# Kernel tuning notes

Hardware: AMD Instinct MI355X
Metric: run time of the kernel (lower is better)

Reference implementation:

```python
import jax, jax.numpy as jnp
import numpy as np

CATS = [1000, 1000, 2000]
NDS = len(CATS)
TOT = sum(CATS)          # total_cats = 4000
N = TOT + NDS            # 4003 source (label) nodes
U = 2048                 # num_unify_class
NFEAT = 256
F = 256                  # nfeat_out
OUT_FEAT = 512           # output_feat_dim
ADJ_FEAT = 256           # adj_feat_dim
SINKHORN_ITERS = 20


def setup_inputs() -> dict:
    key = jax.random.key(0)
    ks = jax.random.split(key, 16)

    def rn(k, shape, s):
        return jax.random.normal(k, shape, dtype=jnp.float32) * s

    return {
        "datasets_node_features": jax.random.normal(ks[0], (TOT, NFEAT), dtype=jnp.float32),
        "unlable_node_features": rn(ks[1], (NDS, NFEAT), 0.02),  # trunc_normal_(std=0.02)
        "adj_matrix": jax.random.uniform(ks[2], (N, U), dtype=jnp.float32),  # torch.rand init
        "W_before": rn(ks[3], (NFEAT, F), 0.05), "b_before": jnp.zeros((F,), jnp.float32),
        "gc1_W": rn(ks[4], (F, F), 0.05), "gc1_b": jnp.zeros((F,), jnp.float32),
        "gc2_W": rn(ks[5], (F, F), 0.05), "gc2_b": jnp.zeros((F,), jnp.float32),
        "gc3_W": rn(ks[6], (F, F), 0.05), "gc3_b": jnp.zeros((F,), jnp.float32),
        "W1": rn(ks[7], (F, OUT_FEAT), 0.05), "b1": jnp.zeros((OUT_FEAT,), jnp.float32),
        "W2": rn(ks[8], (OUT_FEAT, ADJ_FEAT), 0.05), "b2": jnp.zeros((ADJ_FEAT,), jnp.float32),
    }


def _log_optimal_transport(scores, iters):
    # log-space Sinkhorn with uniform marginals 1/(m+n), then rescale by (m+n)
    m, n = scores.shape
    norm = -jnp.log(jnp.asarray(m + n, scores.dtype))
    log_mu = jnp.full((m,), norm, scores.dtype)
    log_nu = jnp.full((n,), norm, scores.dtype)

    def body(carry, _):
        u, v = carry
        u = log_mu - jax.nn.logsumexp(scores + v[None, :], axis=1)
        v = log_nu - jax.nn.logsumexp(scores + u[:, None], axis=0)
        return (u, v), None

    (u, v), _ = jax.lax.scan(body, (jnp.zeros_like(log_mu), jnp.zeros_like(log_nu)),
                             None, length=iters)
    return scores + u[:, None] + v[None, :] - norm


def reference(datasets_node_features, unlable_node_features, adj_matrix,
              W_before, b_before, gc1_W, gc1_b, gc2_W, gc2_b, gc3_W, gc3_b,
              W1, b1, W2, b2):
    # node features: dataset class nodes + per-dataset 'unlabeled' nodes -> [N, NFEAT]
    feats = jnp.concatenate([datasets_node_features, unlable_node_features], axis=0)
    x = jax.nn.relu(feats @ W_before + b_before)  # [N, F]

    # learnable adjacency normalized via differentiable Sinkhorn OT  [N, U]
    A = jnp.exp(_log_optimal_transport(adj_matrix, SINKHORN_ITERS))

    # bipartite message passing: full graph adj has zero diagonal blocks,
    # so spmm(adj, h) splits into A @ h_u (into label nodes) and A.T @ h_n (into unify nodes).
    hn = x                 # [N, F] label-node features
    hu = A.T @ x           # [U, F] initial unify-node features via aggregation

    def gcn(hn, hu, W, b):
        # GraphConvolution: spmm(adj, h @ W) + b ; GCN wrapper: tanh(out + h)
        new_n = jnp.tanh(A @ (hu @ W) + b + hn)
        new_u = jnp.tanh(A.T @ (hn @ W) + b + hu)
        return new_n, new_u

    hn, hu = gcn(hn, hu, gc1_W, gc1_b)
    hn, hu = gcn(hn, hu, gc2_W, gc2_b)
    hn, hu = gcn(hn, hu, gc3_W, gc3_b)

    # output head on unify nodes: linear1 -> relu -> linear2  [U, ADJ_FEAT]
    out = jax.nn.relu(hu @ W1 + b1) @ W2 + b2
    return out
```

## Files before the change

kernel.cpp:

```cpp
#include <hip/hip_runtime.h>
#include <hip/hip_fp16.h>
#include <math.h>

#define NN 4003
#define UU 2048
#define KP 4032
#define N4P 4004
#define NORMC (-8.7079796f)

using bf16x8 = __attribute__((ext_vector_type(8))) short;
using f32x4  = __attribute__((ext_vector_type(4))) float;

#define GLL16(g, l) __builtin_amdgcn_global_load_lds( \
    (const __attribute__((address_space(1))) unsigned*)(g), \
    (__attribute__((address_space(3))) unsigned*)(l), 16, 0, 0)

__device__ __forceinline__ ushort f2bf(float x) {
    unsigned u = __builtin_bit_cast(unsigned, x);
    u += 0x7fff + ((u >> 16) & 1);
    return (ushort)(u >> 16);
}
__device__ __forceinline__ float bf2f(ushort h) {
    unsigned u = ((unsigned)h) << 16;
    return __builtin_bit_cast(float, u);
}
__device__ __forceinline__ void bfsplit(float x, ushort& hi, ushort& lo) {
    hi = f2bf(x);
    lo = f2bf(x - bf2f(hi));
}
__device__ __forceinline__ float h2f(ushort h) {
    return __half2float(__ushort_as_half(h));
}

__global__ void concat_bf(const float* __restrict__ a, const float* __restrict__ b,
                          ushort* __restrict__ fh, ushort* __restrict__ fl) {
    int i = blockIdx.x * 256 + threadIdx.x;
    const int tot4 = NN * 256 / 4;
    if (i >= tot4) return;
    float4 v = (i < 256000) ? ((const float4*)a)[i] : ((const float4*)b)[i - 256000];
    ushort4 hv, lv;
    bfsplit(v.x, hv.x, lv.x); bfsplit(v.y, hv.y, lv.y);
    bfsplit(v.z, hv.z, lv.z); bfsplit(v.w, hv.w, lv.w);
    *(ushort4*)(fh + ((size_t)i << 2)) = hv;
    *(ushort4*)(fl + ((size_t)i << 2)) = lv;
}

__global__ void convW(const float* __restrict__ W, ushort* __restrict__ Th,
                      ushort* __restrict__ Tl, int K, int Nw) {
    __shared__ float tile[32][33];
    int bx = blockIdx.x, by = blockIdx.y;
    int tx = threadIdx.x;
    for (int r = threadIdx.y; r < 32; r += 8)
        tile[r][tx] = W[(size_t)(by * 32 + r) * Nw + bx * 32 + tx];
    __syncthreads();
    for (int r = threadIdx.y; r < 32; r += 8) {
        int n = bx * 32 + r, k = by * 32 + tx;
        ushort hi, lo; bfsplit(tile[tx][r], hi, lo);
        Th[(size_t)n * K + k] = hi;
        Tl[(size_t)n * K + k] = lo;
    }
}

__global__ void conv_sh(const float* __restrict__ S, ushort* __restrict__ Sh) {
    int i = blockIdx.x * 256 + threadIdx.x;
    const int tot4 = NN * UU / 4;
    if (i >= tot4) return;
    float4 s = ((const float4*)S)[i];
    ushort4 h;
    h.x = __half_as_ushort(__float2half(s.x));
    h.y = __half_as_ushort(__float2half(s.y));
    h.z = __half_as_ushort(__float2half(s.z));
    h.w = __half_as_ushort(__float2half(s.w));
    *(ushort4*)(Sh + ((size_t)i << 2)) = h;
}

__global__ void transpose_h(const float* __restrict__ in, ushort* __restrict__ out) {
    __shared__ float tile[32][33];
    int x = blockIdx.x * 32 + threadIdx.x;
    int y0 = blockIdx.y * 32;
    for (int r = threadIdx.y; r < 32; r += 8) {
        int y = y0 + r;
        tile[r][threadIdx.x] = (y < NN) ? in[(size_t)y * UU + x] : 0.0f;
    }
    __syncthreads();
    int oc = y0 + threadIdx.x;
    for (int r = threadIdx.y; r < 32; r += 8) {
        int orow = blockIdx.x * 32 + r;
        out[(size_t)orow * KP + oc] = __half_as_ushort(__float2half(tile[threadIdx.x][r]));
    }
}

__global__ void init_uext(float* __restrict__ u_ext) {
    int i = threadIdx.x;
    if (i < KP - NN) u_ext[NN + i] = -1e30f;
}

__global__ __launch_bounds__(256) void lse2h(const ushort* __restrict__ Sh, int lda,
                                             const float* __restrict__ addv,
                                             float* __restrict__ outv, int C, int R) {
    int r0 = blockIdx.x * 2, r1 = r0 + 1;
    bool has1 = (r1 < R);
    const ushort* rowa = Sh + (size_t)r0 * lda;
    const ushort* rowb = Sh + (size_t)(has1 ? r1 : r0) * lda;
    const float4* a4 = (const float4*)addv;
    float m0 = -INFINITY, s0 = 0.0f, m1 = -INFINITY, s1 = 0.0f;
    int C4 = C >> 2;
    for (int j = threadIdx.x; j < C4; j += 256) {
        float4 av = a4[j];
        ushort4 pa = *(const ushort4*)(rowa + (j << 2));
        ushort4 pb = *(const ushort4*)(rowb + (j << 2));
        float a0 = h2f(pa.x) + av.x, a1 = h2f(pa.y) + av.y;
        float a2 = h2f(pa.z) + av.z, a3 = h2f(pa.w) + av.w;
        float b0 = h2f(pb.x) + av.x, b1 = h2f(pb.y) + av.y;
        float b2 = h2f(pb.z) + av.z, b3 = h2f(pb.w) + av.w;
        float mxa = fmaxf(fmaxf(a0, a1), fmaxf(a2, a3));
        float nm0 = fmaxf(m0, mxa);
        s0 = s0 * __expf(m0 - nm0) + __expf(a0 - nm0) + __expf(a1 - nm0)
                                   + __expf(a2 - nm0) + __expf(a3 - nm0);
        m0 = nm0;
        float mxb = fmaxf(fmaxf(b0, b1), fmaxf(b2, b3));
        float nm1 = fmaxf(m1, mxb);
        s1 = s1 * __expf(m1 - nm1) + __expf(b0 - nm1) + __expf(b1 - nm1)
                                   + __expf(b2 - nm1) + __expf(b3 - nm1);
        m1 = nm1;
    }
    int rem = C & 3;
    if ((int)threadIdx.x < rem) {
        int j = (C4 << 2) + threadIdx.x;
        float av = addv[j];
        float xa = h2f(rowa[j]) + av;
        float nm0 = fmaxf(m0, xa);
        s0 = s0 * __expf(m0 - nm0) + __expf(xa - nm0);
        m0 = nm0;
        float xb = h2f(rowb[j]) + av;
        float nm1 = fmaxf(m1, xb);
        s1 = s1 * __expf(m1 - nm1) + __expf(xb - nm1);
        m1 = nm1;
    }
    #pragma unroll
    for (int off = 1; off < 64; off <<= 1) {
        float om = __shfl_xor(m0, off, 64), os = __shfl_xor(s0, off, 64);
        float nm = fmaxf(m0, om);
        s0 = s0 * __expf(m0 - nm) + os * __expf(om - nm);
        m0 = nm;
        om = __shfl_xor(m1, off, 64); os = __shfl_xor(s1, off, 64);
        nm = fmaxf(m1, om);
        s1 = s1 * __expf(m1 - nm) + os * __expf(om - nm);
        m1 = nm;
    }
    __shared__ float sm[8], ss[8];
    int w = threadIdx.x >> 6;
    if ((threadIdx.x & 63) == 0) { sm[w] = m0; ss[w] = s0; sm[4 + w] = m1; ss[4 + w] = s1; }
    __syncthreads();
    if (threadIdx.x < 2) {
        int b = threadIdx.x * 4;
        float m = sm[b], s = ss[b];
        #pragma unroll
        for (int i = 1; i < 4; ++i) {
            float om = sm[b + i], os = ss[b + i];
            float nm = fmaxf(m, om);
            s = s * __expf(m - nm) + os * __expf(om - nm);
            m = nm;
        }
        int r = r0 + threadIdx.x;
        if (threadIdx.x == 0 || has1) outv[r] = NORMC - (m + __logf(s));
    }
}

__device__ __forceinline__ void exp_row8h(const ushort* __restrict__ Sh,
        const float* __restrict__ rowadd, const float* __restrict__ coladd,
        int lda, int M, int gm, int kbase, uint4& hiv, uint4& lov) {
    ushort h[8], l[8];
    if (gm < M) {
        float ra = rowadd[gm] - NORMC;
        const ushort* rp = Sh + (size_t)gm * lda + kbase;
        ushort4 q0 = *(const ushort4*)rp;
        ushort4 q1 = *(const ushort4*)(rp + 4);
        float4 ca = *(const float4*)(coladd + kbase);
        float4 cb = *(const float4*)(coladd + kbase + 4);
        float vv[8] = {h2f(q0.x) + ca.x, h2f(q0.y) + ca.y, h2f(q0.z) + ca.z, h2f(q0.w) + ca.w,
                       h2f(q1.x) + cb.x, h2f(q1.y) + cb.y, h2f(q1.z) + cb.z, h2f(q1.w) + cb.w};
        #pragma unroll
        for (int e = 0; e < 8; ++e) {
            float av = __expf(vv[e] + ra);
            bfsplit(av, h[e], l[e]);
        }
    } else {
        #pragma unroll
        for (int e = 0; e < 8; ++e) { h[e] = 0; l[e] = 0; }
    }
    hiv.x = (unsigned)h[0] | ((unsigned)h[1] << 16);
    hiv.y = (unsigned)h[2] | ((unsigned)h[3] << 16);
    hiv.z = (unsigned)h[4] | ((unsigned)h[5] << 16);
    hiv.w = (unsigned)h[6] | ((unsigned)h[7] << 16);
    lov.x = (unsigned)l[0] | ((unsigned)l[1] << 16);
    lov.y = (unsigned)l[2] | ((unsigned)l[3] << 16);
    lov.z = (unsigned)l[4] | ((unsigned)l[5] << 16);
    lov.w = (unsigned)l[6] | ((unsigned)l[7] << 16);
}

__global__ __launch_bounds__(512) __attribute__((amdgpu_waves_per_eu(2, 4)))
void gemm_bigN(
        const ushort* __restrict__ Sh, const float* __restrict__ rowadd,
        const float* __restrict__ coladd, int lda,
        const ushort* __restrict__ Bh, const ushort* __restrict__ Bl, int ldb,
        float* __restrict__ P, int M, int K, int Kc) {
    __shared__ __align__(16) ushort SM[2 * 64 * 64 + 2 * 256 * 64];
    ushort* As0 = SM;
    ushort* As1 = SM + 4096;
    ushort* Bs0 = SM + 8192;
    ushort* Bs1 = SM + 8192 + 16384;
    const int tid = threadIdx.x;
    const int bm = blockIdx.x << 6;
    const int lane = tid & 63;
    const int wv = tid >> 6;
    const int wr = (wv >> 2) << 5;
    const int wc = (wv & 3) << 6;
    const int kb = blockIdx.y * Kc;
    int ke = kb + Kc; if (ke > K) ke = K;
    const int arow = tid >> 3, ak8 = (tid & 7) << 3;
    const int as = ((arow << 6) + ak8) ^ ((arow & 7) << 3);
    const int brow_base = wv << 5;
    f32x4 acc[2][4] = {};
    for (int k0 = kb; k0 < ke; k0 += 64) {
        uint4 ah, al;
        exp_row8h(Sh, rowadd, coladd, lda, M, bm + arow, k0 + ak8, ah, al);
        __syncthreads();
        #pragma unroll
        for (int t = 0; t < 4; ++t) {
            int rb2 = brow_base + (t << 3);
            int row = rb2 + (lane >> 3);
            int kksrc = (((lane & 7) ^ (row & 7)) << 3);
            size_t go = (size_t)row * ldb + k0 + kksrc;
            GLL16(Bh + go, &Bs0[rb2 << 6]);
            GLL16(Bl + go, &Bs1[rb2 << 6]);
        }
        *(uint4*)&As0[as] = ah;
        *(uint4*)&As1[as] = al;
        __syncthreads();
        #pragma unroll
        for (int ks = 0; ks < 2; ++ks) {
            int kq = (ks << 5) + ((lane >> 4) << 3);
            bf16x8 fah[2], fal[2], fbh[4], fbl[4];
            #pragma unroll
            for (int f = 0; f < 2; ++f) {
                int rr = wr + (f << 4) + (lane & 15);
                int ia = ((rr << 6) + kq) ^ ((rr & 7) << 3);
                fah[f] = *(const bf16x8*)&As0[ia];
                fal[f] = *(const bf16x8*)&As1[ia];
            }
            #pragma unroll
            for (int g = 0; g < 4; ++g) {
                int cc = wc + (g << 4) + (lane & 15);
                int ib = ((cc << 6) + kq) ^ ((cc & 7) << 3);
                fbh[g] = *(const bf16x8*)&Bs0[ib];
                fbl[g] = *(const bf16x8*)&Bs1[ib];
            }
            #pragma unroll
            for (int i = 0; i < 2; ++i)
                #pragma unroll
                for (int j = 0; j < 4; ++j) {
                    acc[i][j] = __builtin_amdgcn_mfma_f32_16x16x32_bf16(fah[i], fbh[j], acc[i][j], 0, 0, 0);
                    acc[i][j] = __builtin_amdgcn_mfma_f32_16x16x32_bf16(fah[i], fbl[j], acc[i][j], 0, 0, 0);
                    acc[i][j] = __builtin_amdgcn_mfma_f32_16x16x32_bf16(fal[i], fbh[j], acc[i][j], 0, 0, 0);
                }
        }
    }
    __syncthreads();
    float* LF = (float*)SM;
    #pragma unroll
    for (int i = 0; i < 2; ++i) {
        int row0 = wr + (i << 4) + ((lane >> 4) << 2);
        #pragma unroll
        for (int j = 0; j < 4; ++j) {
            int col = wc + (j << 4) + (lane & 15);
            #pragma unroll
            for (int r = 0; r < 4; ++r)
                LF[(row0 + r) * 256 + col] = acc[i][j][r];
        }
    }
    __syncthreads();
    float* Pp = P + (size_t)blockIdx.y * ((size_t)M * 256);
    #pragma unroll
    for (int it = 0; it < 8; ++it) {
        int idx = tid + (it << 9);
        int row = idx >> 6, c4 = (idx & 63) << 2;
        if (bm + row < M)
            *(float4*)(Pp + (size_t)(bm + row) * 256 + c4) = *(const float4*)&LF[row * 256 + c4];
    }
}

__global__ __launch_bounds__(256) __attribute__((amdgpu_waves_per_eu(4, 8)))
void gemm_ks(
        const ushort* __restrict__ Ah, const ushort* __restrict__ Al, int lda,
        const ushort* __restrict__ Bh, const ushort* __restrict__ Bl, int ldb, int Nb,
        float* __restrict__ P, int M, int Nplane, int K, int Kc) {
    __shared__ __align__(16) ushort SM[4 * 64 * 64];
    ushort* As0 = SM;
    ushort* As1 = SM + 4096;
    ushort* Bs0 = SM + 8192;
    ushort* Bs1 = SM + 12288;
    const int tid = threadIdx.x;
    const int bm = blockIdx.y << 6, bn = blockIdx.x << 6;
    const int lane = tid & 63;
    const int wv = tid >> 6;
    const int wm = (wv >> 1) << 5, wn = (wv & 1) << 5;
    const int kb = blockIdx.z * Kc;
    int ke = kb + Kc; if (ke > K) ke = K;
    const int rb = wv << 4;
    f32x4 acc[2][2] = {};
    for (int k0 = kb; k0 < ke; k0 += 64) {
        __syncthreads();
        #pragma unroll
        for (int t = 0; t < 2; ++t) {
            int rb2 = rb + (t << 3);
            int row = rb2 + (lane >> 3);
            int kksrc = (((lane & 7) ^ (row & 7)) << 3);
            int ga = bm + row; ga = (ga < M) ? ga : (M - 1);
            int gb = bn + row; gb = (gb < Nb) ? gb : (Nb - 1);
            size_t goa = (size_t)ga * lda + k0 + kksrc;
            size_t gob = (size_t)gb * ldb + k0 + kksrc;
            GLL16(Ah + goa, &As0[rb2 << 6]);
            GLL16(Al + goa, &As1[rb2 << 6]);
            GLL16(Bh + gob, &Bs0[rb2 << 6]);
            GLL16(Bl + gob, &Bs1[rb2 << 6]);
        }
        __syncthreads();
        #pragma unroll
        for (int ks = 0; ks < 2; ++ks) {
            int kbq = (ks << 5) + ((lane >> 4) << 3);
            bf16x8 fah[2], fal[2], fbh[2], fbl[2];
            #pragma unroll
            for (int f = 0; f < 2; ++f) {
                int rr = wm + (f << 4) + (lane & 15);
                int ia = ((rr << 6) + kbq) ^ ((rr & 7) << 3);
                fah[f] = *(const bf16x8*)&As0[ia];
                fal[f] = *(const bf16x8*)&As1[ia];
                int cc = wn + (f << 4) + (lane & 15);
                int ib = ((cc << 6) + kbq) ^ ((cc & 7) << 3);
                fbh[f] = *(const bf16x8*)&Bs0[ib];
                fbl[f] = *(const bf16x8*)&Bs1[ib];
            }
            #pragma unroll
            for (int i = 0; i < 2; ++i)
                #pragma unroll
                for (int j = 0; j < 2; ++j) {
                    acc[i][j] = __builtin_amdgcn_mfma_f32_16x16x32_bf16(fah[i], fbh[j], acc[i][j], 0, 0, 0);
                    acc[i][j] = __builtin_amdgcn_mfma_f32_16x16x32_bf16(fah[i], fbl[j], acc[i][j], 0, 0, 0);
                    acc[i][j] = __builtin_amdgcn_mfma_f32_16x16x32_bf16(fal[i], fbh[j], acc[i][j], 0, 0, 0);
                }
        }
    }
    __syncthreads();
    float* LF = (float*)SM;
    #pragma unroll
    for (int i = 0; i < 2; ++i) {
        int row0 = wm + (i << 4) + ((lane >> 4) << 2);
        #pragma unroll
        for (int j = 0; j < 2; ++j) {
            int col = wn + (j << 4) + (lane & 15);
            #pragma unroll
            for (int r = 0; r < 4; ++r)
                LF[(row0 + r) * 64 + col] = acc[i][j][r];
        }
    }
    __syncthreads();
    float* Pp = P + (size_t)blockIdx.z * ((size_t)M * Nplane);
    #pragma unroll
    for (int it = 0; it < 4; ++it) {
        int idx = tid + (it << 8);
        int row = idx >> 4, c4 = (idx & 15) << 2;
        if (bm + row < M && bn + c4 < Nplane)
            *(float4*)(Pp + (size_t)(bm + row) * Nplane + bn + c4) = *(const float4*)&LF[row * 64 + c4];
    }
}

template<int ACT, int BIAS, int RES, int OUTK>
__global__ __launch_bounds__(256) void reduce_ks(
        const float* __restrict__ P, int zg,
        const float* __restrict__ bias,
        const ushort* __restrict__ Rh, const ushort* __restrict__ Rl,
        float* __restrict__ Cf, ushort* __restrict__ Ch, ushort* __restrict__ Cl,
        int M, int N4, int ldo) {
    int t = blockIdx.x * 256 + threadIdx.x;
    int n4w = N4 >> 2;
    int tot = M * n4w;
    if (t >= tot) return;
    int m = t / n4w;
    int n = (t - m * n4w) << 2;
    size_t pstr = (size_t)M * N4;
    const float* base = P + (size_t)m * N4 + n;
    float4 a = *(const float4*)base;
    for (int z = 1; z < zg; ++z) {
        float4 b = *(const float4*)(base + (size_t)z * pstr);
        a.x += b.x; a.y += b.y; a.z += b.z; a.w += b.w;
    }
    if (BIAS == 1) {
        float4 bv = *(const float4*)(bias + n);
        a.x += bv.x; a.y += bv.y; a.z += bv.z; a.w += bv.w;
    }
    if (BIAS == 2) {
        float s = bias[m];
        a.x += s; a.y += s; a.z += s; a.w += s;
    }
    if (RES) {
        size_t ro = (size_t)m * ldo + n;
        ushort4 rh = *(const ushort4*)(Rh + ro);
        ushort4 rl = *(const ushort4*)(Rl + ro);
        a.x += bf2f(rh.x) + bf2f(rl.x); a.y += bf2f(rh.y) + bf2f(rl.y);
        a.z += bf2f(rh.z) + bf2f(rl.z); a.w += bf2f(rh.w) + bf2f(rl.w);
    }
    if (ACT == 1) {
        a.x = fmaxf(a.x, 0.f); a.y = fmaxf(a.y, 0.f);
        a.z = fmaxf(a.z, 0.f); a.w = fmaxf(a.w, 0.f);
    }
    if (ACT == 2) {
        a.x = tanhf(a.x); a.y = tanhf(a.y); a.z = tanhf(a.z); a.w = tanhf(a.w);
    }
    size_t co = (size_t)m * ldo + n;
    if (OUTK == 0) {
        *(float4*)(Cf + co) = a;
    } else {
        ushort4 hv, lv;
        bfsplit(a.x, hv.x, lv.x); bfsplit(a.y, hv.y, lv.y);
        bfsplit(a.z, hv.z, lv.z); bfsplit(a.w, hv.w, lv.w);
        *(ushort4*)(Ch + co) = hv;
        *(ushort4*)(Cl + co) = lv;
    }
}

static inline int rgrid(int M, int N4) { return (M * (N4 >> 2) + 255) / 256; }

extern "C" void kernel_launch(void* const* d_in, const int* in_sizes, int n_in,
                              void* d_out, int out_size, void* d_ws, size_t ws_size,
                              hipStream_t stream) {
    const float* dsf = (const float*)d_in[0];
    const float* unl = (const float*)d_in[1];
    const float* S   = (const float*)d_in[2];
    const float* Wb  = (const float*)d_in[3];
    const float* bb  = (const float*)d_in[4];
    const float* gcW[3] = {(const float*)d_in[5], (const float*)d_in[7], (const float*)d_in[9]};
    const float* gcb[3] = {(const float*)d_in[6], (const float*)d_in[8], (const float*)d_in[10]};
    const float* W1 = (const float*)d_in[11];
    const float* b1 = (const float*)d_in[12];
    const float* W2 = (const float*)d_in[13];
    const float* b2 = (const float*)d_in[14];
    float* out = (float*)d_out;

    char* p = (char*)d_ws;
    ushort* Shm = (ushort*)p; p += (size_t)NN * UU * 2;
    ushort* STh = (ushort*)p; p += (size_t)UU * KP * 2;
    float* P    = (float*)p;  p += (size_t)8 * NN * 256 * 4;
    ushort* fh = (ushort*)p; ushort* fl = fh + (size_t)NN * 256; p += (size_t)NN * 256 * 4;
    ushort* xh = (ushort*)p; ushort* xl = xh + (size_t)NN * 256; p += (size_t)NN * 256 * 4;
    ushort* xTh = (ushort*)p; ushort* xTl = xTh + (size_t)256 * KP; p += (size_t)256 * KP * 4;
    ushort* huh = (ushort*)p; ushort* hul = huh + (size_t)UU * 256; p += (size_t)UU * 256 * 4;
    ushort* tuTh = (ushort*)p; ushort* tuTl = tuTh + (size_t)256 * UU; p += (size_t)256 * UU * 4;
    ushort* tnTh = (ushort*)p; ushort* tnTl = tnTh + (size_t)256 * KP; p += (size_t)256 * KP * 4;
    float* u_ext = (float*)p; p += KP * 4;
    float* v     = (float*)p; p += UU * 4;
    ushort* WbTh = (ushort*)p; ushort* WbTl = WbTh + 256 * 256; p += 256 * 256 * 4;
    ushort* gWh[3]; ushort* gWl[3];
    for (int l = 0; l < 3; ++l) { gWh[l] = (ushort*)p; gWl[l] = gWh[l] + 256 * 256; p += 256 * 256 * 4; }
    ushort* W1Th = (ushort*)p; ushort* W1Tl = W1Th + 512 * 256; p += 512 * 256 * 4;
    ushort* W2Th = (ushort*)p; ushort* W2Tl = W2Th + 256 * 512; p += 256 * 512 * 4;
    ushort* h1h = xh; ushort* h1l = h1h + (size_t)UU * 512;
    (void)ws_size;

    concat_bf<<<dim3(1001), dim3(256), 0, stream>>>(dsf, unl, fh, fl);
    convW<<<dim3(8, 8),  dim3(32, 8), 0, stream>>>(Wb, WbTh, WbTl, 256, 256);
    for (int l = 0; l < 3; ++l)
        convW<<<dim3(8, 8), dim3(32, 8), 0, stream>>>(gcW[l], gWh[l], gWl[l], 256, 256);
    convW<<<dim3(16, 8), dim3(32, 8), 0, stream>>>(W1, W1Th, W1Tl, 256, 512);
    convW<<<dim3(8, 16), dim3(32, 8), 0, stream>>>(W2, W2Th, W2Tl, 512, 256);
    init_uext<<<dim3(1), dim3(64), 0, stream>>>(u_ext);
    conv_sh<<<dim3((NN * UU / 4 + 255) / 256), dim3(256), 0, stream>>>(S, Shm);
    transpose_h<<<dim3(64, 126), dim3(32, 8), 0, stream>>>(S, STh);
    hipMemsetAsync(v, 0, UU * sizeof(float), stream);

    gemm_ks<<<dim3(4, 63, 4), 256, 0, stream>>>(
        fh, fl, 256, WbTh, WbTl, 256, 256, P, NN, 256, 256, 64);
    reduce_ks<1,1,0,1><<<rgrid(NN,256), 256, 0, stream>>>(
        P, 4, bb, nullptr, nullptr, nullptr, xh, xl, NN, 256, 256);
    gemm_ks<<<dim3(63, 4, 4), 256, 0, stream>>>(
        WbTh, WbTl, 256, fh, fl, 256, NN, P, 256, N4P, 256, 64);
    reduce_ks<1,2,0,1><<<rgrid(256,N4P), 256, 0, stream>>>(
        P, 4, bb, nullptr, nullptr, nullptr, xTh, xTl, 256, N4P, KP);

    for (int it = 0; it < 20; ++it) {
        lse2h<<<dim3((NN + 1) / 2), dim3(256), 0, stream>>>(Shm, UU, v, u_ext, UU, NN);
        lse2h<<<dim3(UU / 2),       dim3(256), 0, stream>>>(STh, KP, u_ext, v, NN, UU);
    }

    gemm_bigN<<<dim3(32, 8), 512, 0, stream>>>(
        STh, v, u_ext, KP, xTh, xTl, KP, P, UU, KP, 512);
    reduce_ks<0,0,0,1><<<rgrid(UU,256), 256, 0, stream>>>(
        P, 8, nullptr, nullptr, nullptr, nullptr, huh, hul, UU, 256, 256);

    for (int l = 0; l < 3; ++l) {
        const ushort* hnh = (l == 0) ? xh : fh;
        const ushort* hnl = (l == 0) ? xl : fl;
        if (l < 2) {
            gemm_ks<<<dim3(32, 4, 4), 256, 0, stream>>>(
                gWh[l], gWl[l], 256, huh, hul, 256, UU, P, 256, UU, 256, 64);
            reduce_ks<0,0,0,1><<<rgrid(256,UU), 256, 0, stream>>>(
                P, 4, nullptr, nullptr, nullptr, nullptr, tuTh, tuTl, 256, UU, UU);
        }
        gemm_ks<<<dim3(63, 4, 4), 256, 0, stream>>>(
            gWh[l], gWl[l], 256, hnh, hnl, 256, NN, P, 256, N4P, 256, 64);
        reduce_ks<0,0,0,1><<<rgrid(256,N4P), 256, 0, stream>>>(
            P, 4, nullptr, nullptr, nullptr, nullptr, tnTh, tnTl, 256, N4P, KP);
        if (l < 2) {
            gemm_bigN<<<dim3(63, 8), 512, 0, stream>>>(
                Shm, u_ext, v, UU, tuTh, tuTl, UU, P, NN, UU, 256);
            reduce_ks<2,1,1,1><<<rgrid(NN,256), 256, 0, stream>>>(
                P, 8, gcb[l], hnh, hnl, nullptr, fh, fl, NN, 256, 256);
        }
        gemm_bigN<<<dim3(32, 8), 512, 0, stream>>>(
            STh, v, u_ext, KP, tnTh, tnTl, KP, P, UU, KP, 512);
        reduce_ks<2,1,1,1><<<rgrid(UU,256), 256, 0, stream>>>(
            P, 8, gcb[l], huh, hul, nullptr, huh, hul, UU, 256, 256);
    }

    gemm_ks<<<dim3(8, 32, 4), 256, 0, stream>>>(
        huh, hul, 256, W1Th, W1Tl, 256, 512, P, UU, 512, 256, 64);
    reduce_ks<1,1,0,1><<<rgrid(UU,512), 256, 0, stream>>>(
        P, 4, b1, nullptr, nullptr, nullptr, h1h, h1l, UU, 512, 512);
    gemm_ks<<<dim3(4, 32, 8), 256, 0, stream>>>(
        h1h, h1l, 512, W2Th, W2Tl, 512, 256, P, UU, 256, 512, 64);
    reduce_ks<0,1,0,0><<<rgrid(UU,256), 256, 0, stream>>>(
        P, 8, b2, nullptr, nullptr, out, nullptr, nullptr, UU, 256, 256);
}
```

Measured before the change: 591.6 us.

## Fuse Sinkhorn iterations into one cooperative kernel with LDS-resident score tiles

Replaces the 40 separate row/column logsumexp launches with a single cooperative kernel of 512 blocks. Each block loads its 8 rows of the fp16 score matrix and 4 rows of its transpose into shared memory once and keeps them there for all 20 iterations, using grid-wide syncs between the row and column half-steps. This removes repeated global reads of the score matrix and the per-launch overhead. In exchange it needs about 64KB of LDS per block, all blocks co-resident, and 40 grid barriers, and it leaves fewer waves per row for the reduction.

Result: slower. 2.359 ms (+298.7%).

```diff
diff --git a/kernel.cpp b/kernel.cpp
--- a/kernel.cpp
+++ b/kernel.cpp
@@ -1,6 +1,9 @@
 #include <hip/hip_runtime.h>
 #include <hip/hip_fp16.h>
+#include <hip/hip_cooperative_groups.h>
 #include <math.h>
+
+namespace cg = cooperative_groups;
 
 #define NN 4003
 #define UU 2048
@@ -95,75 +98,91 @@
     if (i < KP - NN) u_ext[NN + i] = -1e30f;
 }
 
-__global__ __launch_bounds__(256) void lse2h(const ushort* __restrict__ Sh, int lda,
-                                             const float* __restrict__ addv,
-                                             float* __restrict__ outv, int C, int R) {
-    int r0 = blockIdx.x * 2, r1 = r0 + 1;
-    bool has1 = (r1 < R);
-    const ushort* rowa = Sh + (size_t)r0 * lda;
-    const ushort* rowb = Sh + (size_t)(has1 ? r1 : r0) * lda;
-    const float4* a4 = (const float4*)addv;
-    float m0 = -INFINITY, s0 = 0.0f, m1 = -INFINITY, s1 = 0.0f;
-    int C4 = C >> 2;
-    for (int j = threadIdx.x; j < C4; j += 256) {
-        float4 av = a4[j];
-        ushort4 pa = *(const ushort4*)(rowa + (j << 2));
-        ushort4 pb = *(const ushort4*)(rowb + (j << 2));
-        float a0 = h2f(pa.x) + av.x, a1 = h2f(pa.y) + av.y;
-        float a2 = h2f(pa.z) + av.z, a3 = h2f(pa.w) + av.w;
-        float b0 = h2f(pb.x) + av.x, b1 = h2f(pb.y) + av.y;
-        float b2 = h2f(pb.z) + av.z, b3 = h2f(pb.w) + av.w;
-        float mxa = fmaxf(fmaxf(a0, a1), fmaxf(a2, a3));
-        float nm0 = fmaxf(m0, mxa);
-        s0 = s0 * __expf(m0 - nm0) + __expf(a0 - nm0) + __expf(a1 - nm0)
-                                   + __expf(a2 - nm0) + __expf(a3 - nm0);
-        m0 = nm0;
-        float mxb = fmaxf(fmaxf(b0, b1), fmaxf(b2, b3));
-        float nm1 = fmaxf(m1, mxb);
-        s1 = s1 * __expf(m1 - nm1) + __expf(b0 - nm1) + __expf(b1 - nm1)
-                                   + __expf(b2 - nm1) + __expf(b3 - nm1);
-        m1 = nm1;
-    }
-    int rem = C & 3;
-    if ((int)threadIdx.x < rem) {
-        int j = (C4 << 2) + threadIdx.x;
-        float av = addv[j];
-        float xa = h2f(rowa[j]) + av;
-        float nm0 = fmaxf(m0, xa);
-        s0 = s0 * __expf(m0 - nm0) + __expf(xa - nm0);
-        m0 = nm0;
-        float xb = h2f(rowb[j]) + av;
-        float nm1 = fmaxf(m1, xb);
-        s1 = s1 * __expf(m1 - nm1) + __expf(xb - nm1);
-        m1 = nm1;
-    }
+__device__ __forceinline__ void lse8(uint4 pk, float4 a0, float4 a1, float& m, float& s) {
+    float x0 = h2f((ushort)(pk.x & 0xffff)) + a0.x;
+    float x1 = h2f((ushort)(pk.x >> 16))    + a0.y;
+    float x2 = h2f((ushort)(pk.y & 0xffff)) + a0.z;
+    float x3 = h2f((ushort)(pk.y >> 16))    + a0.w;
+    float x4 = h2f((ushort)(pk.z & 0xffff)) + a1.x;
+    float x5 = h2f((ushort)(pk.z >> 16))    + a1.y;
+    float x6 = h2f((ushort)(pk.w & 0xffff)) + a1.z;
+    float x7 = h2f((ushort)(pk.w >> 16))    + a1.w;
+    float mx = fmaxf(fmaxf(fmaxf(x0, x1), fmaxf(x2, x3)),
+                     fmaxf(fmaxf(x4, x5), fmaxf(x6, x7)));
+    float nm = fmaxf(m, mx);
+    s = s * __expf(m - nm)
+        + __expf(x0 - nm) + __expf(x1 - nm) + __expf(x2 - nm) + __expf(x3 - nm)
+        + __expf(x4 - nm) + __expf(x5 - nm) + __expf(x6 - nm) + __expf(x7 - nm);
+    m = nm;
+}
+__device__ __forceinline__ void wave_lse_reduce(float& m, float& s) {
     #pragma unroll
     for (int off = 1; off < 64; off <<= 1) {
-        float om = __shfl_xor(m0, off, 64), os = __shfl_xor(s0, off, 64);
-        float nm = fmaxf(m0, om);
-        s0 = s0 * __expf(m0 - nm) + os * __expf(om - nm);
-        m0 = nm;
-        om = __shfl_xor(m1, off, 64); os = __shfl_xor(s1, off, 64);
-        nm = fmaxf(m1, om);
-        s1 = s1 * __expf(m1 - nm) + os * __expf(om - nm);
-        m1 = nm;
-    }
-    __shared__ float sm[8], ss[8];
-    int w = threadIdx.x >> 6;
-    if ((threadIdx.x & 63) == 0) { sm[w] = m0; ss[w] = s0; sm[4 + w] = m1; ss[4 + w] = s1; }
-    __syncthreads();
-    if (threadIdx.x < 2) {
-        int b = threadIdx.x * 4;
-        float m = sm[b], s = ss[b];
-        #pragma unroll
-        for (int i = 1; i < 4; ++i) {
-            float om = sm[b + i], os = ss[b + i];
-            float nm = fmaxf(m, om);
-            s = s * __expf(m - nm) + os * __expf(om - nm);
-            m = nm;
-        }
-        int r = r0 + threadIdx.x;
-        if (threadIdx.x == 0 || has1) outv[r] = NORMC - (m + __logf(s));
+        float om = __shfl_xor(m, off, 64), os = __shfl_xor(s, off, 64);
+        float nm = fmaxf(m, om);
+        s = s * __expf(m - nm) + os * __expf(om - nm);
+        m = nm;
+    }
+}
+
+__global__ __launch_bounds__(256) void sinkhorn_coop(
+        const ushort* __restrict__ Shm, const ushort* __restrict__ STh,
+        float* __restrict__ u_ext, float* __restrict__ v) {
+    __shared__ __align__(16) ushort Ls[8 * 2048 + 4 * 4032];
+    ushort* Lr = Ls;
+    ushort* Lc = Ls + 8 * 2048;
+    cg::grid_group grid = cg::this_grid();
+    const int b = blockIdx.x, tid = threadIdx.x;
+    const int r0 = b << 3;
+    const int c0 = b << 2;
+    for (int i = tid; i < 2048; i += 256) {
+        int row = i >> 8, off = (i & 255) << 3;
+        int g = r0 + row;
+        uint4 vls = {0, 0, 0, 0};
+        if (g < NN) vls = *(const uint4*)(Shm + (size_t)g * 2048 + off);
+        *(uint4*)&Lr[(row << 11) + off] = vls;
+    }
+    for (int i = tid; i < 2016; i += 256) {
+        int row = i / 504, off = (i - row * 504) << 3;
+        *(uint4*)&Lc[row * 4032 + off] = *(const uint4*)(STh + (size_t)(c0 + row) * 4032 + off);
+    }
+    __syncthreads();
+    const int wave = tid >> 6, lane = tid & 63;
+    for (int it = 0; it < 20; ++it) {
+        #pragma unroll
+        for (int q = 0; q < 2; ++q) {
+            int rr = (wave << 1) + q;
+            int g = r0 + rr;
+            float m = -INFINITY, s = 0.0f;
+            #pragma unroll
+            for (int c = 0; c < 4; ++c) {
+                int j0 = (c << 9) + (lane << 3);
+                uint4 pk = *(const uint4*)&Lr[(rr << 11) + j0];
+                float4 a0 = *(const float4*)(v + j0);
+                float4 a1 = *(const float4*)(v + j0 + 4);
+                lse8(pk, a0, a1, m, s);
+            }
+            wave_lse_reduce(m, s);
+            if (lane == 0 && g < NN) u_ext[g] = NORMC - (m + __logf(s));
+        }
+        grid.sync();
+        {
+            int g = c0 + wave;
+            float m = -INFINITY, s = 0.0f;
+            #pragma unroll
+            for (int c = 0; c < 8; ++c) {
+                int j0 = (c << 9) + (lane << 3);
+                if (j0 < 4032) {
+                    uint4 pk = *(const uint4*)&Lc[wave * 4032 + j0];
+                    float4 a0 = *(const float4*)(u_ext + j0);
+                    float4 a1 = *(const float4*)(u_ext + j0 + 4);
+                    lse8(pk, a0, a1, m, s);
+                }
+            }
+            wave_lse_reduce(m, s);
+            if (lane == 0) v[g] = NORMC - (m + __logf(s));
+        }
+        grid.sync();
     }
 }
 
@@ -487,9 +506,10 @@
     reduce_ks<1,2,0,1><<<rgrid(256,N4P), 256, 0, stream>>>(
         P, 4, bb, nullptr, nullptr, nullptr, xTh, xTl, 256, N4P, KP);
 
-    for (int it = 0; it < 20; ++it) {
-        lse2h<<<dim3((NN + 1) / 2), dim3(256), 0, stream>>>(Shm, UU, v, u_ext, UU, NN);
-        lse2h<<<dim3(UU / 2),       dim3(256), 0, stream>>>(STh, KP, u_ext, v, NN, UU);
+    {
+        void* args[] = {(void*)&Shm, (void*)&STh, (void*)&u_ext, (void*)&v};
+        hipLaunchCooperativeKernel((void*)sinkhorn_coop, dim3(512), dim3(256),
+                                   args, 0, stream);
     }
 
     gemm_bigN<<<dim3(32, 8), 512, 0, stream>>>(
```
